# Optimization experiments

Measured on AMD Instinct MI355X. Metric: run time of the kernel, lower is better.

The kernel has to match this reference:

```python
import jax, jax.numpy as jnp
import numpy as np

V = 50257
D = 512
T = 1024


def setup_inputs() -> dict:
    key = jax.random.key(0)
    ks = jax.random.split(key, 12)
    si = (2.0 / (V + D)) ** 0.5   # xavier-ish scale for input matrices
    sh = (1.0 / D) ** 0.5         # scale for recurrent matrices
    so = (2.0 / (V + D)) ** 0.5
    return {
        "idx": jax.random.randint(ks[0], (T,), 0, V, dtype=jnp.int32),
        "W_ii": jax.random.normal(ks[1], (D, V), jnp.float32) * si,
        "W_if": jax.random.normal(ks[2], (D, V), jnp.float32) * si,
        "W_io": jax.random.normal(ks[3], (D, V), jnp.float32) * si,
        "W_ig": jax.random.normal(ks[4], (D, V), jnp.float32) * si,
        "W_hi": jax.random.normal(ks[5], (D, D), jnp.float32) * sh,
        "W_hf": jax.random.normal(ks[6], (D, D), jnp.float32) * sh,
        "W_ho": jax.random.normal(ks[7], (D, D), jnp.float32) * sh,
        "W_hg": jax.random.normal(ks[8], (D, D), jnp.float32) * sh,
        "b_i": jnp.zeros((D,), jnp.float32),
        "b_f": jnp.ones((D,), jnp.float32),
        "b_o": jnp.zeros((D,), jnp.float32),
        "b_g": jnp.zeros((D,), jnp.float32),
        "W_out": jax.random.normal(ks[9], (V, D), jnp.float32) * so,
        "b_out": jnp.zeros((V,), jnp.float32),
    }


def reference(idx, W_ii, W_if, W_io, W_ig, W_hi, W_hf, W_ho, W_hg,
              b_i, b_f, b_o, b_g, W_out, b_out):
    # One-hot @ W.T == column gather: W[:, tok]. Dropout is identity (eval mode).
    dims = W_hi.shape[0]

    def step(carry, tok):
        h, c = carry
        i = jax.nn.sigmoid(W_ii[:, tok] + b_i + W_hi @ h)
        f = jax.nn.sigmoid(W_if[:, tok] + b_f + W_hf @ h)
        o = jax.nn.sigmoid(W_io[:, tok] + b_o + W_ho @ h)
        g = jnp.tanh(W_ig[:, tok] + b_g + W_hg @ h)
        c_new = f * c + i * g
        h_new = o * jnp.tanh(c_new)
        logits = W_out @ h_new + b_out          # [V]
        return (h_new, c_new), jax.nn.log_softmax(logits)

    h0 = jnp.zeros((dims,), W_hi.dtype)
    c0 = jnp.zeros((dims,), W_hi.dtype)
    (h, c), log_probs = jax.lax.scan(step, (h0, c0), idx)
    return log_probs, h, c  # log_probs: [T, V]
```

## Files before the change

kernel.cpp:

```cpp
#include <hip/hip_runtime.h>
#include <hip/hip_bf16.h>

#define VV 50257
#define DD 512
#define TT 1024
#define VPADN 50304
#define NBR 64
#define WCB 128

typedef __bf16 bf16;
typedef __attribute__((ext_vector_type(8))) __bf16 bf16x8;
typedef __attribute__((ext_vector_type(4))) __bf16 bf16x4;
typedef __attribute__((ext_vector_type(4))) float f32x4;

__device__ __forceinline__ void gload_lds16(const void* g, void* l) {
  __builtin_amdgcn_global_load_lds(
      (__attribute__((address_space(1))) void*)(void*)g,
      (__attribute__((address_space(3))) void*)l, 16, 0, 0);
}

__global__ __launch_bounds__(512) __attribute__((amdgpu_waves_per_eu(2, 2)))
void recur_fused_kernel(
    const int* __restrict__ idx,
    const float* __restrict__ Wii, const float* __restrict__ Wif,
    const float* __restrict__ Wio, const float* __restrict__ Wig,
    const float* __restrict__ Whi, const float* __restrict__ Whf,
    const float* __restrict__ Who, const float* __restrict__ Whg,
    const float* __restrict__ bi, const float* __restrict__ bfv,
    const float* __restrict__ bo, const float* __restrict__ bg,
    const float* __restrict__ Wout,
    unsigned long long* __restrict__ Hpack, bf16* __restrict__ Hbf,
    bf16* __restrict__ Wbf, float* __restrict__ out_tail) {
  __shared__ float hsh[2][DD];
  __shared__ int idxs[TT];
  const int b = blockIdx.x, tid = threadIdx.x;

  if (b >= NBR) {
    const int wb = b - NBR;
    const size_t nch = (size_t)VPADN * DD / 4;
    for (size_t i = (size_t)wb * 512 + tid; i < nch; i += (size_t)WCB * 512) {
      size_t e = i << 2;
      bf16x4 o;
      if ((e >> 9) < VV) {
        f32x4 x = *(const f32x4*)&Wout[e];
        o[0] = (bf16)x[0]; o[1] = (bf16)x[1]; o[2] = (bf16)x[2]; o[3] = (bf16)x[3];
      } else {
        o[0] = o[1] = o[2] = o[3] = (bf16)0.f;
      }
      *(bf16x4*)&Wbf[e] = o;
    }
    return;
  }

  idxs[tid] = idx[tid];
  idxs[tid + 512] = idx[tid + 512];

  const int lane = tid & 63, w = tid >> 6;
  const int hd = (b << 3) + w;

  f32x4 wr0[4], wr1[4];
  {
    #pragma unroll
    for (int gg = 0; gg < 4; ++gg) {
      const float* Wg = (gg == 0) ? Whi : (gg == 1) ? Whf : (gg == 2) ? Who : Whg;
      wr0[gg] = *(const f32x4*)&Wg[(size_t)hd*DD + (lane << 2)];
      wr1[gg] = *(const f32x4*)&Wg[(size_t)hd*DD + 256 + (lane << 2)];
    }
  }
  #pragma unroll
  for (int gg = 0; gg < 4; ++gg) {
    asm volatile("" : "+v"(wr0[gg]));
    asm volatile("" : "+v"(wr1[gg]));
  }

  const float* wxp = nullptr;
  float bias = 0.f;
  if (lane < 4) {
    const float* Wx = (lane == 0) ? Wii : (lane == 1) ? Wif : (lane == 2) ? Wio : Wig;
    const float* bx = (lane == 0) ? bi : (lane == 1) ? bfv : (lane == 2) ? bo : bg;
    wxp = &Wx[(size_t)hd * VV];
    bias = bx[hd];
  }
  float c = 0.f, hout = 0.f;
  __syncthreads();

  for (int t = 0; t < TT; ++t) {
    float xv = 0.f;
    if (lane < 4) xv = wxp[idxs[t]] + bias;

    float* hb = hsh[t & 1];
    if (t > 0) {
      const unsigned long long* src = &Hpack[(size_t)(t-1)*DD + tid];
      unsigned long long v;
      do {
        asm volatile("global_load_dwordx2 %0, %1, off sc1\n\t"
                     "s_waitcnt vmcnt(0)"
                     : "=v"(v) : "v"(src) : "memory");
      } while (__builtin_expect((unsigned)(v >> 32) != (unsigned)t, 0));
      hb[tid] = __uint_as_float((unsigned)v);
    } else {
      hb[tid] = 0.f;
    }
    __syncthreads();

    const f32x4 h0 = *(const f32x4*)&hb[lane << 2];
    const f32x4 h1 = *(const f32x4*)&hb[256 + (lane << 2)];
    f32x4 m0 = wr0[0]*h0 + wr1[0]*h1;
    f32x4 m1 = wr0[1]*h0 + wr1[1]*h1;
    f32x4 m2 = wr0[2]*h0 + wr1[2]*h1;
    f32x4 m3 = wr0[3]*h0 + wr1[3]*h1;
    float a0 = m0[0]+m0[1]+m0[2]+m0[3];
    float a1 = m1[0]+m1[1]+m1[2]+m1[3];
    float a2 = m2[0]+m2[1]+m2[2]+m2[3];
    float a3 = m3[0]+m3[1]+m3[2]+m3[3];
    #pragma unroll
    for (int mask = 1; mask < 64; mask <<= 1) {
      a0 += __shfl_xor(a0, mask);
      a1 += __shfl_xor(a1, mask);
      a2 += __shfl_xor(a2, mask);
      a3 += __shfl_xor(a3, mask);
    }

    float myacc = (lane == 0) ? a0 : (lane == 1) ? a1 : (lane == 2) ? a2 : a3;
    float pre = myacc + xv;
    bool isg = (lane == 3);
    float e1 = __expf(isg ? -2.f * pre : -pre);
    float rr = 1.f / (1.f + e1);
    float act = isg ? (2.f * rr - 1.f) : rr;

    float ia = __shfl(act, 0);
    float fa = __shfl(act, 1);
    float oa = __shfl(act, 2);
    float ga = __shfl(act, 3);

    if (lane == 0) {
      c = fa * c + ia * ga;
      float e2 = __expf(-2.f * c);
      float th = 2.f / (1.f + e2) - 1.f;
      hout = oa * th;
      unsigned long long pk =
          ((unsigned long long)(unsigned)(t + 1) << 32) |
          (unsigned long long)__float_as_uint(hout);
      __hip_atomic_store(&Hpack[(size_t)t*DD + hd], pk, __ATOMIC_RELAXED,
                         __HIP_MEMORY_SCOPE_AGENT);
      Hbf[(size_t)t*DD + hd] = (bf16)hout;
      if (t == TT - 1) { out_tail[hd] = hout; out_tail[DD + hd] = c; }
    }
  }
}

__global__ __launch_bounds__(256, 2) void gemm_kernel(
    const bf16* __restrict__ A, const bf16* __restrict__ B,
    const float* __restrict__ bout, float* __restrict__ Cout) {
  __shared__ bf16 As[128*32];
  __shared__ bf16 Bs[128*32];
  __shared__ float Cs[4][16][72];
  const int tid = threadIdx.x;
  const int n0 = blockIdx.x * 128, m0 = blockIdx.y * 128;
  const int w = tid >> 6, l = tid & 63;
  const int wr = w >> 1, wc = w & 1;
  f32x4 acc[4][4] = {};

  for (int k0 = 0; k0 < DD; k0 += 32) {
    #pragma unroll
    for (int c = 0; c < 2; ++c) {
      int j = c*256 + tid;
      int row = j >> 2, kc = (j & 3) << 3;
      gload_lds16(&A[(size_t)(m0 + row)*DD + k0 + kc], (char*)As + (c*4096 + w*1024));
      gload_lds16(&B[(size_t)(n0 + row)*DD + k0 + kc], (char*)Bs + (c*4096 + w*1024));
    }
    __syncthreads();
    bf16x8 af[4], bfr[4];
    #pragma unroll
    for (int mi = 0; mi < 4; ++mi)
      af[mi] = *(const bf16x8*)&As[(wr*64 + mi*16 + (l & 15))*32 + (l >> 4)*8];
    #pragma unroll
    for (int ni = 0; ni < 4; ++ni)
      bfr[ni] = *(const bf16x8*)&Bs[(wc*64 + ni*16 + (l & 15))*32 + (l >> 4)*8];
    #pragma unroll
    for (int mi = 0; mi < 4; ++mi)
      #pragma unroll
      for (int ni = 0; ni < 4; ++ni)
        acc[mi][ni] = __builtin_amdgcn_mfma_f32_16x16x32_bf16(af[mi], bfr[ni], acc[mi][ni], 0, 0, 0);
    __syncthreads();
  }

  float bbv[4];
  #pragma unroll
  for (int ni = 0; ni < 4; ++ni) {
    int col = n0 + wc*64 + ni*16 + (l & 15);
    bbv[ni] = (col < VV) ? bout[col] : 0.f;
  }

  #pragma unroll
  for (int mi = 0; mi < 4; ++mi) {
    #pragma unroll
    for (int ni = 0; ni < 4; ++ni)
      #pragma unroll
      for (int r = 0; r < 4; ++r)
        Cs[w][(l >> 4)*4 + r][ni*16 + (l & 15)] = acc[mi][ni][r] + bbv[ni];
    const int rbase = m0 + wr*64 + mi*16;
    #pragma unroll
    for (int i = 0; i < 4; ++i) {
      int idx2 = i*64 + l;
      int row = idx2 >> 4, quad = idx2 & 15;
      int col = n0 + wc*64 + quad*4;
      f32x4 v = *(const f32x4*)&Cs[w][row][quad*4];
      float* dst = &Cout[(size_t)(rbase + row)*VV + col];
      if (col + 3 < VV) {
        asm volatile("global_store_dwordx4 %0, %1, off"
                     :: "v"(dst), "v"(v) : "memory");
      } else {
        #pragma unroll
        for (int e = 0; e < 4; ++e)
          if (col + e < VV) dst[e] = v[e];
      }
    }
  }
}

__global__ __launch_bounds__(512) void lsm_kernel(float* __restrict__ logits) {
  const int t = blockIdx.x, tid = threadIdx.x;
  float* row = logits + (size_t)t*VV;
  const size_t base = (size_t)t * VV;
  const int head = (int)((4 - (base & 3)) & 3);
  const int nvec = (VV - head) >> 2;
  const int tail0 = head + (nvec << 2);

  float m = -INFINITY, s = 0.f;
  if (tid < head) {
    float x = row[tid];
    m = x; s = 1.f;
  } else if (tid >= 508 && (tail0 + (tid - 508)) < VV) {
    float x = row[tail0 + (tid - 508)];
    m = x; s = 1.f;
  }
  for (int i = tid; i < nvec; i += 512) {
    f32x4 x = *(const f32x4*)&row[head + (i << 2)];
    float mx = fmaxf(fmaxf(x[0], x[1]), fmaxf(x[2], x[3]));
    float nm = fmaxf(m, mx);
    s = s*__expf(m - nm) + __expf(x[0] - nm) + __expf(x[1] - nm)
        + __expf(x[2] - nm) + __expf(x[3] - nm);
    m = nm;
  }
  #pragma unroll
  for (int mask = 1; mask < 64; mask <<= 1) {
    float om = __shfl_xor(m, mask);
    float os = __shfl_xor(s, mask);
    float nm = fmaxf(m, om);
    s = s*__expf(m - nm) + os*__expf(om - nm);
    m = nm;
  }
  __shared__ float sm[8], ss[8], lse_sh;
  int wv = tid >> 6;
  if ((tid & 63) == 0) { sm[wv] = m; ss[wv] = s; }
  __syncthreads();
  if (tid == 0) {
    float M = sm[0], S = ss[0];
    for (int i2 = 1; i2 < 8; ++i2) {
      float nm = fmaxf(M, sm[i2]);
      S = S*__expf(M - nm) + ss[i2]*__expf(sm[i2] - nm);
      M = nm;
    }
    lse_sh = M + logf(S);
  }
  __syncthreads();
  float lse = lse_sh;
  if (tid < head) row[tid] -= lse;
  else if (tid >= 508 && (tail0 + (tid - 508)) < VV) row[tail0 + (tid - 508)] -= lse;
  for (int i = tid; i < nvec; i += 512) {
    float* p = &row[head + (i << 2)];
    f32x4 x = *(const f32x4*)p;
    x[0] -= lse; x[1] -= lse; x[2] -= lse; x[3] -= lse;
    *(f32x4*)p = x;
  }
}

extern "C" void kernel_launch(void* const* d_in, const int* in_sizes, int n_in,
                              void* d_out, int out_size, void* d_ws, size_t ws_size,
                              hipStream_t stream) {
  const int*   idx  = (const int*)d_in[0];
  const float* Wii  = (const float*)d_in[1];
  const float* Wif  = (const float*)d_in[2];
  const float* Wio  = (const float*)d_in[3];
  const float* Wig  = (const float*)d_in[4];
  const float* Whi  = (const float*)d_in[5];
  const float* Whf  = (const float*)d_in[6];
  const float* Who  = (const float*)d_in[7];
  const float* Whg  = (const float*)d_in[8];
  const float* bi   = (const float*)d_in[9];
  const float* bfv  = (const float*)d_in[10];
  const float* bo   = (const float*)d_in[11];
  const float* bg   = (const float*)d_in[12];
  const float* Wout = (const float*)d_in[13];
  const float* bout = (const float*)d_in[14];
  float* out = (float*)d_out;

  char* ws = (char*)d_ws;
  bf16*  Wbf  = (bf16*)ws;
  unsigned long long* Hpack = (unsigned long long*)(ws + 51511296);
  bf16*  Hbf  = (bf16*)(ws + 55705600);

  hipMemsetAsync(Hpack, 0, (size_t)TT*DD*8, stream);
  recur_fused_kernel<<<NBR + WCB, 512, 0, stream>>>(
      idx, Wii, Wif, Wio, Wig, Whi, Whf, Who, Whg, bi, bfv, bo, bg, Wout,
      Hpack, Hbf, Wbf, out + (size_t)TT*VV);
  gemm_kernel<<<dim3(393, 8), 256, 0, stream>>>(Hbf, Wbf, bout, out);
  lsm_kernel<<<TT, 512, 0, stream>>>(out);
}
```

Before: 1.980 ms.

## Compute per-tile softmax max/sum in GEMM epilogue; LSM only subtracts LSE

The GEMM epilogue now reduces each 128-column tile to a per-row max and sum-of-exp partial, written to workspace. The log-softmax kernel merges the 393 partials per row instead of re-reading the full logits row, which removes one full pass over the ~200MB logits tensor. The cost is extra shuffles, exps and a block barrier per mi iteration in the GEMM epilogue. Separately, a short s_sleep is inserted before the recurrent kernel's polling loop to reduce spin pressure on memory.

Result: slower. 2.127 ms (+7.4%).

```diff
diff --git a/kernel.cpp b/kernel.cpp
--- a/kernel.cpp
+++ b/kernel.cpp
@@ -7,6 +7,7 @@
 #define VPADN 50304
 #define NBR 64
 #define WCB 128
+#define PSTR 400
 
 typedef __bf16 bf16;
 typedef __attribute__((ext_vector_type(8))) __bf16 bf16x8;
@@ -90,6 +91,7 @@
 
     float* hb = hsh[t & 1];
     if (t > 0) {
+      __builtin_amdgcn_s_sleep(8);
       const unsigned long long* src = &Hpack[(size_t)(t-1)*DD + tid];
       unsigned long long v;
       do {
@@ -151,12 +153,16 @@
 
 __global__ __launch_bounds__(256, 2) void gemm_kernel(
     const bf16* __restrict__ A, const bf16* __restrict__ B,
-    const float* __restrict__ bout, float* __restrict__ Cout) {
+    const float* __restrict__ bout, float* __restrict__ Cout,
+    float* __restrict__ Pmax, float* __restrict__ Psum) {
   __shared__ bf16 As[128*32];
   __shared__ bf16 Bs[128*32];
   __shared__ float Cs[4][16][72];
+  __shared__ float partm[2][2][16];
+  __shared__ float parts[2][2][16];
   const int tid = threadIdx.x;
-  const int n0 = blockIdx.x * 128, m0 = blockIdx.y * 128;
+  const int nb = blockIdx.x;
+  const int n0 = nb * 128, m0 = blockIdx.y * 128;
   const int w = tid >> 6, l = tid & 63;
   const int wr = w >> 1, wc = w & 1;
   f32x4 acc[4][4] = {};
@@ -186,10 +192,12 @@
   }
 
   float bbv[4];
+  bool colok[4];
   #pragma unroll
   for (int ni = 0; ni < 4; ++ni) {
     int col = n0 + wc*64 + ni*16 + (l & 15);
-    bbv[ni] = (col < VV) ? bout[col] : 0.f;
+    colok[ni] = (col < VV);
+    bbv[ni] = colok[ni] ? bout[col] : 0.f;
   }
 
   #pragma unroll
@@ -199,6 +207,35 @@
       #pragma unroll
       for (int r = 0; r < 4; ++r)
         Cs[w][(l >> 4)*4 + r][ni*16 + (l & 15)] = acc[mi][ni][r] + bbv[ni];
+
+    #pragma unroll
+    for (int r = 0; r < 4; ++r) {
+      float v0 = colok[0] ? acc[mi][0][r] + bbv[0] : -1e30f;
+      float v1 = colok[1] ? acc[mi][1][r] + bbv[1] : -1e30f;
+      float v2 = colok[2] ? acc[mi][2][r] + bbv[2] : -1e30f;
+      float v3 = colok[3] ? acc[mi][3][r] + bbv[3] : -1e30f;
+      float pm = fmaxf(fmaxf(v0, v1), fmaxf(v2, v3));
+      #pragma unroll
+      for (int mk = 1; mk < 16; mk <<= 1) pm = fmaxf(pm, __shfl_xor(pm, mk));
+      float ps = __expf(v0 - pm) + __expf(v1 - pm) + __expf(v2 - pm) + __expf(v3 - pm);
+      #pragma unroll
+      for (int mk = 1; mk < 16; mk <<= 1) ps += __shfl_xor(ps, mk);
+      if ((l & 15) == 0) {
+        partm[wr][wc][(l >> 4)*4 + r] = pm;
+        parts[wr][wc][(l >> 4)*4 + r] = ps;
+      }
+    }
+    __syncthreads();
+    if (tid < 32) {
+      int wr2 = tid >> 4, row16 = tid & 15;
+      float ma = partm[wr2][0][row16], mb = partm[wr2][1][row16];
+      float M = fmaxf(ma, mb);
+      float S = parts[wr2][0][row16]*__expf(ma - M) + parts[wr2][1][row16]*__expf(mb - M);
+      int gr = m0 + wr2*64 + mi*16 + row16;
+      Pmax[(size_t)gr*PSTR + nb] = M;
+      Psum[(size_t)gr*PSTR + nb] = S;
+    }
+
     const int rbase = m0 + wr*64 + mi*16;
     #pragma unroll
     for (int i = 0; i < 4; ++i) {
@@ -216,32 +253,20 @@
           if (col + e < VV) dst[e] = v[e];
       }
     }
-  }
-}
-
-__global__ __launch_bounds__(512) void lsm_kernel(float* __restrict__ logits) {
+    __syncthreads();
+  }
+}
+
+__global__ __launch_bounds__(512) void lsm_kernel(float* __restrict__ logits,
+                                                  const float* __restrict__ Pmax,
+                                                  const float* __restrict__ Psum) {
   const int t = blockIdx.x, tid = threadIdx.x;
   float* row = logits + (size_t)t*VV;
-  const size_t base = (size_t)t * VV;
-  const int head = (int)((4 - (base & 3)) & 3);
-  const int nvec = (VV - head) >> 2;
-  const int tail0 = head + (nvec << 2);
-
-  float m = -INFINITY, s = 0.f;
-  if (tid < head) {
-    float x = row[tid];
-    m = x; s = 1.f;
-  } else if (tid >= 508 && (tail0 + (tid - 508)) < VV) {
-    float x = row[tail0 + (tid - 508)];
-    m = x; s = 1.f;
-  }
-  for (int i = tid; i < nvec; i += 512) {
-    f32x4 x = *(const f32x4*)&row[head + (i << 2)];
-    float mx = fmaxf(fmaxf(x[0], x[1]), fmaxf(x[2], x[3]));
-    float nm = fmaxf(m, mx);
-    s = s*__expf(m - nm) + __expf(x[0] - nm) + __expf(x[1] - nm)
-        + __expf(x[2] - nm) + __expf(x[3] - nm);
-    m = nm;
+
+  float m = -1e30f, s = 0.f;
+  if (tid < 393) {
+    m = Pmax[(size_t)t*PSTR + tid];
+    s = Psum[(size_t)t*PSTR + tid];
   }
   #pragma unroll
   for (int mask = 1; mask < 64; mask <<= 1) {
@@ -265,7 +290,12 @@
     lse_sh = M + logf(S);
   }
   __syncthreads();
-  float lse = lse_sh;
+  const float lse = lse_sh;
+
+  const size_t base = (size_t)t * VV;
+  const int head = (int)((4 - (base & 3)) & 3);
+  const int nvec = (VV - head) >> 2;
+  const int tail0 = head + (nvec << 2);
   if (tid < head) row[tid] -= lse;
   else if (tid >= 508 && (tail0 + (tid - 508)) < VV) row[tail0 + (tid - 508)] -= lse;
   for (int i = tid; i < nvec; i += 512) {
@@ -300,11 +330,13 @@
   bf16*  Wbf  = (bf16*)ws;
   unsigned long long* Hpack = (unsigned long long*)(ws + 51511296);
   bf16*  Hbf  = (bf16*)(ws + 55705600);
+  float* Pmax = (float*)(ws + 56754176);
+  float* Psum = (float*)(ws + 58392576);
 
   hipMemsetAsync(Hpack, 0, (size_t)TT*DD*8, stream);
   recur_fused_kernel<<<NBR + WCB, 512, 0, stream>>>(
       idx, Wii, Wif, Wio, Wig, Whi, Whf, Who, Whg, bi, bfv, bo, bg, Wout,
       Hpack, Hbf, Wbf, out + (size_t)TT*VV);
-  gemm_kernel<<<dim3(393, 8), 256, 0, stream>>>(Hbf, Wbf, bout, out);
-  lsm_kernel<<<TT, 512, 0, stream>>>(out);
-}
+  gemm_kernel<<<dim3(393, 8), 256, 0, stream>>>(Hbf, Wbf, bout, out, Pmax, Psum);
+  lsm_kernel<<<TT, 512, 0, stream>>>(out, Pmax, Psum);
+}
```
